# Performance work log

Hardware: AMD Instinct MI355X
Metric: run time of the kernel (lower is better)

The kernel has to match this reference:

```python
import jax, jax.numpy as jnp
import numpy as np

N, E, D, H = 50000, 500000, 128, 128


def setup_inputs() -> dict:
    key = jax.random.key(0)
    ks = jax.random.split(key, 20)
    s = 0.05
    inp = {
        "node_states": jax.random.normal(ks[0], (N, D), jnp.float32),
        "edge_features": jax.random.normal(ks[1], (E, D), jnp.float32),
        "from_idx": jax.random.randint(ks[2], (E,), 0, N, dtype=jnp.int32),
        "to_idx": jax.random.randint(ks[3], (E,), 0, N, dtype=jnp.int32),
        "graph_idx": jax.random.randint(ks[4], (N,), 0, 16, dtype=jnp.int32),
        # message MLP: Linear(3D,H)-ReLU-Linear(H,H)-ReLU-Linear(H,D)
        "mW1": jax.random.normal(ks[5], (3 * D, H), jnp.float32) * s,
        "mb1": jnp.zeros((H,), jnp.float32),
        "mW2": jax.random.normal(ks[6], (H, H), jnp.float32) * s,
        "mb2": jnp.zeros((H,), jnp.float32),
        "mW3": jax.random.normal(ks[7], (H, D), jnp.float32) * s,
        "mb3": jnp.zeros((D,), jnp.float32),
    }
    # three GRU cells; W: input->gates [D,3D], U: hidden->gates [D,3D]; gate order r,z,n (torch)
    for i, g in enumerate(["g0", "g1", "g2"]):
        inp[g + "W"] = jax.random.normal(ks[8 + 2 * i], (D, 3 * D), jnp.float32) * s
        inp[g + "U"] = jax.random.normal(ks[9 + 2 * i], (D, 3 * D), jnp.float32) * s
        inp[g + "b"] = jnp.zeros((3 * D,), jnp.float32)
        inp[g + "c"] = jnp.zeros((3 * D,), jnp.float32)
    return inp


def _mlp(x, W1, b1, W2, b2, W3, b3):
    h = jax.nn.relu(x @ W1 + b1)
    h = jax.nn.relu(h @ W2 + b2)
    return h @ W3 + b3


def _gru(x, h, W, U, b, c):
    gi = x @ W + b  # [N,3D]
    gh = h @ U + c
    ir, iz, inn = jnp.split(gi, 3, axis=1)
    hr, hz, hn = jnp.split(gh, 3, axis=1)
    r = jax.nn.sigmoid(ir + hr)
    z = jax.nn.sigmoid(iz + hz)
    n = jnp.tanh(inn + r * hn)
    return (1.0 - z) * n + z * h


def reference(node_states, edge_features, from_idx, to_idx, graph_idx,
              mW1, mb1, mW2, mb2, mW3, mb3,
              g0W, g0U, g0b, g0c, g1W, g1U, g1b, g1c, g2W, g2U, g2b, g2c):
    n_nodes = node_states.shape[0]

    def prop_once(fi, ti):
        edge_in = jnp.concatenate(
            [node_states[fi], node_states[ti], edge_features], axis=1)  # [E,3D]
        edge_states = _mlp(edge_in, mW1, mb1, mW2, mb2, mW3, mb3)  # [E,D]
        return jax.ops.segment_sum(edge_states, ti, num_segments=n_nodes)

    # forward uses self.message_net for BOTH directions (reverse net unused)
    agg = prop_once(from_idx, to_idx) + prop_once(to_idx, from_idx)  # [N,D]

    h1 = _gru(node_states, agg, g0W, g0U, g0b, g0c)
    h2 = _gru(agg, h1, g1W, g1U, g1b, g1c)
    h3 = _gru(h1, h2, g2W, g2U, g2b, g2c)
    return h3
```

## Files before the change

### kernel.cpp

```cpp
#include <hip/hip_runtime.h>

typedef unsigned short u16;
typedef __attribute__((ext_vector_type(8))) short bf16x8;
typedef __attribute__((ext_vector_type(4))) float f32x4;

__device__ inline u16 f2bf(float f) {
  unsigned int u = __float_as_uint(f);
  u += 0x7fffu + ((u >> 16) & 1u);
  return (u16)(u >> 16);
}
__device__ inline float bf2f(u16 v) {
  return __uint_as_float((unsigned)v << 16);
}

__device__ inline uint4 pack8(float4 a, float4 b) {
  uint4 r;
  r.x = (unsigned)f2bf(a.x) | ((unsigned)f2bf(a.y) << 16);
  r.y = (unsigned)f2bf(a.z) | ((unsigned)f2bf(a.w) << 16);
  r.z = (unsigned)f2bf(b.x) | ((unsigned)f2bf(b.y) << 16);
  r.w = (unsigned)f2bf(b.z) | ((unsigned)f2bf(b.w) << 16);
  return r;
}

struct TransDesc {
  const float* src[9];
  u16* dst[9];
  int R[9];
  int C[9];
  int pre[10];
};

__global__ void transpose_all_kernel(TransDesc td) {
  int t = blockIdx.x * 256 + threadIdx.x;
  if (t >= td.pre[9]) return;
  int seg = 0;
  while (t >= td.pre[seg + 1]) ++seg;
  int local = t - td.pre[seg];
  int C = td.C[seg], R = td.R[seg];
  int r = local / C, c = local - r * C;
  td.dst[seg][(size_t)c * R + r] = f2bf(td.src[seg][local]);
}

__global__ void count_kernel(const int* __restrict__ fi,
                             const int* __restrict__ ti,
                             int* __restrict__ cnt, int E) {
  int e = blockIdx.x * 256 + threadIdx.x;
  if (e < E) {
    atomicAdd(&cnt[ti[e]], 1);
    atomicAdd(&cnt[fi[e]], 1);
  }
}

__global__ void scan1_kernel(const int* __restrict__ cnt,
                             int* __restrict__ partial, int N, int chunk) {
  __shared__ int sdata[256];
  int b = blockIdx.x, t = threadIdx.x;
  int base = b * chunk;
  int sum = 0;
  for (int i = t; i < chunk; i += 256) {
    int idx = base + i;
    if (idx < N) sum += cnt[idx];
  }
  sdata[t] = sum;
  __syncthreads();
  for (int s2 = 128; s2 > 0; s2 >>= 1) {
    if (t < s2) sdata[t] += sdata[t + s2];
    __syncthreads();
  }
  if (t == 0) partial[b] = sdata[0];
}

__global__ void scan2_kernel(int* __restrict__ partial) {
  __shared__ int s[256];
  int t = threadIdx.x;
  int own = partial[t];
  s[t] = own;
  __syncthreads();
  for (int d2 = 1; d2 < 256; d2 <<= 1) {
    int v = (t >= d2) ? s[t - d2] : 0;
    __syncthreads();
    s[t] += v;
    __syncthreads();
  }
  partial[t] = s[t] - own;
}

__global__ void scan3_kernel(const int* __restrict__ cnt,
                             const int* __restrict__ partialEx,
                             int* __restrict__ cursor, int N, int chunk) {
  __shared__ int s[256];
  int b = blockIdx.x, t = threadIdx.x;
  int base = b * chunk;
  int own = (t < chunk && base + t < N) ? cnt[base + t] : 0;
  s[t] = own;
  __syncthreads();
  for (int d2 = 1; d2 < 256; d2 <<= 1) {
    int v = (t >= d2) ? s[t - d2] : 0;
    __syncthreads();
    s[t] += v;
    __syncthreads();
  }
  int ex = s[t] - own + partialEx[b];
  if (t < chunk && base + t < N) cursor[base + t] = ex;
}

__global__ void slot_kernel(const int* __restrict__ fi,
                            const int* __restrict__ ti,
                            int* __restrict__ cursor, int* __restrict__ s_nbr,
                            int* __restrict__ s_eid, int* __restrict__ s_dest,
                            int E) {
  int e = blockIdx.x * 256 + threadIdx.x;
  if (e < E) {
    int f = fi[e], t2 = ti[e];
    int p0 = atomicAdd(&cursor[t2], 1);
    s_nbr[p0] = f;
    s_eid[p0] = e;
    s_dest[p0] = t2;
    int p1 = atomicAdd(&cursor[f], 1);
    s_nbr[p1] = t2;
    s_eid[p1] = e;
    s_dest[p1] = f;
  }
}

__device__ inline void stage_w_rw(u16* sW, const u16* __restrict__ src,
                                  int roww, int colofs, int tid) {
  int n = tid >> 1, half = tid & 1;
  const u16* s = src + (size_t)n * roww + colofs + half * 64;
#pragma unroll
  for (int q = 0; q < 8; ++q) {
    uint4 v = *(const uint4*)(s + q * 8);
    int byte = n * 256 + ((half * 128 + q * 16) ^ ((n & 7) << 4));
    *(uint4*)((char*)sW + byte) = v;
  }
}

__device__ inline void mfma_pass(const u16* A, const u16* W, f32x4 acc[8],
                                 int w, int lane) {
  const int cA = lane & 15;
  const int ko = (lane >> 4) * 8;
  const int arow = 16 * w + cA;
#pragma unroll
  for (int kk = 0; kk < 4; ++kk) {
    int ka = (kk * 32 + ko) * 2;
    int sx = ka ^ ((cA & 7) << 4);
    bf16x8 a = *(const bf16x8*)((const char*)A + arow * 256 + sx);
#pragma unroll
    for (int nt = 0; nt < 8; ++nt) {
      bf16x8 bb = *(const bf16x8*)((const char*)W + (nt * 16 + cA) * 256 + sx);
      acc[nt] = __builtin_amdgcn_mfma_f32_16x16x32_bf16(a, bb, acc[nt], 0, 0, 0);
    }
  }
}

__device__ inline void write_h_lds(u16* sH, const f32x4 acc[8], int w,
                                   int lane) {
#pragma unroll
  for (int nt = 0; nt < 8; ++nt) {
    int col = nt * 16 + (lane & 15);
#pragma unroll
    for (int i = 0; i < 4; ++i) {
      int rr = 16 * w + ((lane >> 4) * 4) + i;
      *(u16*)((char*)sH + rr * 256 + ((col * 2) ^ ((rr & 7) << 4))) =
          f2bf(acc[nt][i]);
    }
  }
}

__global__ __launch_bounds__(256) void node_partial_kernel(
    const float* __restrict__ ns, const u16* __restrict__ Wt1,
    u16* __restrict__ Pa, u16* __restrict__ Pb, int N) {
  __shared__ u16 sA[64 * 128];
  __shared__ u16 sW[128 * 128];
  const int tid = threadIdx.x;
  const int lane = tid & 63;
  const int w = tid >> 6;
  const int r0 = blockIdx.x * 64;
  {
    int row = tid >> 2, seg = tid & 3;
    int rr = r0 + row;
    if (rr >= N) rr = N - 1;
    const float4* sx = (const float4*)(ns + (size_t)rr * 128 + seg * 32);
#pragma unroll
    for (int q = 0; q < 4; ++q) {
      int byte = row * 256 + ((seg * 64 + q * 16) ^ ((row & 7) << 4));
      *(uint4*)((char*)sA + byte) = pack8(sx[q * 2], sx[q * 2 + 1]);
    }
  }
  stage_w_rw(sW, Wt1, 384, 0, tid);
  __syncthreads();
  f32x4 accA[8] = {};
  mfma_pass(sA, sW, accA, w, lane);
  __syncthreads();
  stage_w_rw(sW, Wt1, 384, 128, tid);
  __syncthreads();
  f32x4 accB[8] = {};
  mfma_pass(sA, sW, accB, w, lane);
#pragma unroll
  for (int nt = 0; nt < 8; ++nt) {
    int col = nt * 16 + (lane & 15);
#pragma unroll
    for (int i = 0; i < 4; ++i) {
      int rr = 16 * w + ((lane >> 4) * 4) + i;
      int row = r0 + rr;
      if (row < N) {
        Pa[(size_t)row * 128 + col] = f2bf(accA[nt][i]);
        Pb[(size_t)row * 128 + col] = f2bf(accB[nt][i]);
      }
    }
  }
}

__global__ __launch_bounds__(256) void efgemm_kernel(
    const float* __restrict__ ef, const u16* __restrict__ Wt1,
    const float* __restrict__ b1, u16* __restrict__ EFm, int E) {
  __shared__ u16 sA[64 * 128];
  __shared__ u16 sW[128 * 128];
  const int tid = threadIdx.x;
  const int lane = tid & 63;
  const int w = tid >> 6;
  const int r0 = blockIdx.x * 64;
  {
    int row = tid >> 2, seg = tid & 3;
    int rr = r0 + row;
    if (rr >= E) rr = E - 1;
    const float4* sx = (const float4*)(ef + (size_t)rr * 128 + seg * 32);
#pragma unroll
    for (int q = 0; q < 4; ++q) {
      int byte = row * 256 + ((seg * 64 + q * 16) ^ ((row & 7) << 4));
      *(uint4*)((char*)sA + byte) = pack8(sx[q * 2], sx[q * 2 + 1]);
    }
  }
  stage_w_rw(sW, Wt1, 384, 256, tid);
  __syncthreads();
  f32x4 acc[8] = {};
  mfma_pass(sA, sW, acc, w, lane);
  __syncthreads();
#pragma unroll
  for (int nt = 0; nt < 8; ++nt) {
    int col = nt * 16 + (lane & 15);
    float bv = b1[col];
#pragma unroll
    for (int i = 0; i < 4; ++i) {
      int rr = 16 * w + ((lane >> 4) * 4) + i;
      *(u16*)((char*)sA + rr * 256 + ((col * 2) ^ ((rr & 7) << 4))) =
          f2bf(acc[nt][i] + bv);
    }
  }
  __syncthreads();
#pragma unroll
  for (int it = 0; it < 4; ++it) {
    int task = tid + (it << 8);
    int row = task >> 4, c8 = task & 15;
    int gr = r0 + row;
    if (gr < E) {
      uint4 v = *(const uint4*)((const char*)sA + row * 256 +
                                ((c8 << 4) ^ ((row & 7) << 4)));
      *(uint4*)(EFm + (size_t)gr * 128 + (c8 << 3)) = v;
    }
  }
}

__global__ __launch_bounds__(512, 2) void edge_csr_kernel(
    const u16* __restrict__ EFm, const int* __restrict__ s_nbr,
    const int* __restrict__ s_eid, const int* __restrict__ s_dest,
    const u16* __restrict__ Wt2, const u16* __restrict__ Wt3,
    const u16* __restrict__ Pa, const u16* __restrict__ Pb,
    const float* __restrict__ b2, const float* __restrict__ b3,
    float* __restrict__ aggf, int nslots, int ntiles) {
  __shared__ u16 sH[128 * 128];
  __shared__ int sNbr[128];
  __shared__ int sEid[128];
  __shared__ int sDest[128];
  const int tid = threadIdx.x;
  const int lane = tid & 63;
  const int wv = tid >> 6;
  const int mw = wv >> 1;
  const int nw = wv & 1;
  const int l15 = lane & 15;
  const int lhi = lane >> 4;

  float b2f[4], b3f[4];
#pragma unroll
  for (int nt = 0; nt < 4; ++nt) {
    int col = (nw << 6) + (nt << 4) + l15;
    b2f[nt] = b2[col];
    b3f[nt] = b3[col];
  }
  bf16x8 w2f[4][4], w3f[4][4];
#pragma unroll
  for (int nt = 0; nt < 4; ++nt) {
    int c = (nw << 6) + (nt << 4) + l15;
#pragma unroll
    for (int kk = 0; kk < 4; ++kk) {
      w2f[nt][kk] = *(const bf16x8*)(Wt2 + (size_t)c * 128 + (kk << 5) + (lhi << 3));
      w3f[nt][kk] = *(const bf16x8*)(Wt3 + (size_t)c * 128 + (kk << 5) + (lhi << 3));
    }
  }
  __syncthreads();

  for (int t = blockIdx.x; t < ntiles; t += gridDim.x) {
    const int r0 = t << 7;
    if (tid < 128) {
      int r = r0 + tid;
      int rc = r < nslots ? r : nslots - 1;
      sNbr[tid] = s_nbr[rc];
      sEid[tid] = s_eid[rc];
      sDest[tid] = (r < nslots) ? s_dest[rc] : -1;
    }
    __syncthreads();
#pragma unroll
    for (int it = 0; it < 4; ++it) {
      int row = (tid >> 4) + (it << 5);
      int c8 = tid & 15;
      int nbr = sNbr[row], eid = sEid[row];
      int dst = sDest[row];
      if (dst < 0) dst = 0;
      uint4 efv = *(const uint4*)(EFm + (size_t)eid * 128 + (c8 << 3));
      uint4 pav = *(const uint4*)(Pa + (size_t)nbr * 128 + (c8 << 3));
      uint4 pbv = *(const uint4*)(Pb + (size_t)dst * 128 + (c8 << 3));
      const u16* pe = (const u16*)&efv;
      const u16* pa = (const u16*)&pav;
      const u16* pb = (const u16*)&pbv;
      unsigned o[4];
#pragma unroll
      for (int j = 0; j < 4; ++j) {
        float v0 = fmaxf(bf2f(pe[2 * j]) + bf2f(pa[2 * j]) + bf2f(pb[2 * j]), 0.f);
        float v1 = fmaxf(bf2f(pe[2 * j + 1]) + bf2f(pa[2 * j + 1]) + bf2f(pb[2 * j + 1]), 0.f);
        o[j] = (unsigned)f2bf(v0) | ((unsigned)f2bf(v1) << 16);
      }
      *(uint4*)((char*)sH + row * 256 + ((c8 << 4) ^ ((row & 7) << 4))) = *(uint4*)o;
    }
    __syncthreads();
    bf16x8 hA[2][4];
#pragma unroll
    for (int m = 0; m < 2; ++m) {
      int ra = (mw << 5) + (m << 4) + l15;
#pragma unroll
      for (int kk = 0; kk < 4; ++kk) {
        int sx = ((kk << 6) + (lhi << 4)) ^ ((ra & 7) << 4);
        hA[m][kk] = *(const bf16x8*)((const char*)sH + ra * 256 + sx);
      }
    }
    f32x4 acc2[2][4] = {};
#pragma unroll
    for (int kk = 0; kk < 4; ++kk)
#pragma unroll
      for (int nt = 0; nt < 4; ++nt)
#pragma unroll
        for (int m = 0; m < 2; ++m)
          acc2[m][nt] = __builtin_amdgcn_mfma_f32_16x16x32_bf16(
              hA[m][kk], w2f[nt][kk], acc2[m][nt], 0, 0, 0);
    __syncthreads();
#pragma unroll
    for (int m = 0; m < 2; ++m) {
#pragma unroll
      for (int i = 0; i < 4; ++i) {
        int rl = (mw << 5) + (m << 4) + (lhi << 2) + i;
#pragma unroll
        for (int nt = 0; nt < 4; ++nt) {
          int col = (nw << 6) + (nt << 4) + l15;
          float v = fmaxf(acc2[m][nt][i] + b2f[nt], 0.f);
          *(u16*)((char*)sH + rl * 256 + ((col * 2) ^ ((rl & 7) << 4))) = f2bf(v);
        }
      }
    }
    __syncthreads();
#pragma unroll
    for (int m = 0; m < 2; ++m) {
      int ra = (mw << 5) + (m << 4) + l15;
#pragma unroll
      for (int kk = 0; kk < 4; ++kk) {
        int sx = ((kk << 6) + (lhi << 4)) ^ ((ra & 7) << 4);
        hA[m][kk] = *(const bf16x8*)((const char*)sH + ra * 256 + sx);
      }
    }
    f32x4 acc3[2][4] = {};
#pragma unroll
    for (int kk = 0; kk < 4; ++kk)
#pragma unroll
      for (int nt = 0; nt < 4; ++nt)
#pragma unroll
        for (int m = 0; m < 2; ++m)
          acc3[m][nt] = __builtin_amdgcn_mfma_f32_16x16x32_bf16(
              hA[m][kk], w3f[nt][kk], acc3[m][nt], 0, 0, 0);
    __syncthreads();
#pragma unroll
    for (int m = 0; m < 2; ++m) {
#pragma unroll
      for (int i = 0; i < 4; ++i) {
        int rl = (mw << 5) + (m << 4) + (lhi << 2) + i;
#pragma unroll
        for (int nt = 0; nt < 4; ++nt) {
          int col = (nw << 6) + (nt << 4) + l15;
          *(u16*)((char*)sH + rl * 256 + ((col * 2) ^ ((rl & 7) << 4))) =
              f2bf(acc3[m][nt][i] + b3f[nt]);
        }
      }
    }
    __syncthreads();
    {
      int c = tid & 127, q = tid >> 7;
      float s = 0.f;
      int prev = -1;
      int rbeg = q << 5;
#pragma unroll 4
      for (int rr = rbeg; rr < rbeg + 32; ++rr) {
        int d = sDest[rr];
        if (d != prev) {
          if (prev >= 0) unsafeAtomicAdd(&aggf[(size_t)prev * 128 + c], s);
          prev = d;
          s = 0.f;
        }
        if (d >= 0)
          s += bf2f(*(const u16*)((const char*)sH + rr * 256 +
                                  ((c * 2) ^ ((rr & 7) << 4))));
      }
      if (prev >= 0) unsafeAtomicAdd(&aggf[(size_t)prev * 128 + c], s);
    }
    __syncthreads();
  }
}

__global__ __launch_bounds__(256, 2) void gru3_kernel(
    const float* __restrict__ ns, const float* __restrict__ aggf,
    const u16* __restrict__ g0W, const u16* __restrict__ g0U,
    const u16* __restrict__ g1W, const u16* __restrict__ g1U,
    const u16* __restrict__ g2W, const u16* __restrict__ g2U,
    const float* __restrict__ b0, const float* __restrict__ c0,
    const float* __restrict__ b1, const float* __restrict__ c1,
    const float* __restrict__ b2, const float* __restrict__ c2,
    float* __restrict__ out, int N) {
  __shared__ u16 sX[64 * 128];
  __shared__ u16 sG[64 * 128];
  __shared__ u16 sW[128 * 128];
  const int tid = threadIdx.x;
  const int lane = tid & 63;
  const int w = tid >> 6;
  const int r0 = blockIdx.x * 64;
  {
    int row = tid >> 2, seg = tid & 3;
    int rr = r0 + row;
    if (rr >= N) rr = N - 1;
    const float4* sx = (const float4*)(ns + (size_t)rr * 128 + seg * 32);
    const float4* sh = (const float4*)(aggf + (size_t)rr * 128 + seg * 32);
#pragma unroll
    for (int q = 0; q < 4; ++q) {
      int byte = row * 256 + ((seg * 64 + q * 16) ^ ((row & 7) << 4));
      *(uint4*)((char*)sX + byte) = pack8(sx[q * 2], sx[q * 2 + 1]);
      *(uint4*)((char*)sG + byte) = pack8(sh[q * 2], sh[q * 2 + 1]);
    }
  }

  float hpf[8][4];

#define GPASS(SRC, ABUF, ACC)                       \
  __syncthreads();                                  \
  stage_w_rw(sW, (SRC), 128, 0, tid);               \
  __syncthreads();                                  \
  mfma_pass((ABUF), sW, (ACC), w, lane);

  {
    f32x4 ar[8] = {}, az[8] = {}, ai[8] = {}, ah[8] = {};
    GPASS(g0W + 0 * 16384, sX, ar)
    GPASS(g0U + 0 * 16384, sG, ar)
    GPASS(g0W + 1 * 16384, sX, az)
    GPASS(g0U + 1 * 16384, sG, az)
    GPASS(g0W + 2 * 16384, sX, ai)
    GPASS(g0U + 2 * 16384, sG, ah)
    f32x4 h1[8];
#pragma unroll
    for (int nt = 0; nt < 8; ++nt) {
      int col = nt * 16 + (lane & 15);
      float brc = b0[col] + c0[col];
      float bzc = b0[128 + col] + c0[128 + col];
      float bi = b0[256 + col];
      float bc2 = c0[256 + col];
#pragma unroll
      for (int i = 0; i < 4; ++i) {
        int rloc = 16 * w + ((lane >> 4) * 4) + i;
        int row = r0 + rloc;
        int rowc = row < N ? row : N - 1;
        float hf = aggf[(size_t)rowc * 128 + col];
        float rg = 1.f / (1.f + __expf(-(ar[nt][i] + brc)));
        float zg = 1.f / (1.f + __expf(-(az[nt][i] + bzc)));
        float pre = ai[nt][i] + bi + rg * (ah[nt][i] + bc2);
        float ng = 2.f / (1.f + __expf(-2.f * pre)) - 1.f;
        float hv = (1.f - zg) * ng + zg * hf;
        h1[nt][i] = hv;
        hpf[nt][i] = hv;
      }
    }
    write_h_lds(sX, h1, w, lane);
  }
  {
    f32x4 ar[8] = {}, az[8] = {}, ai[8] = {}, ah[8] = {};
    GPASS(g1W + 0 * 16384, sG, ar)
    GPASS(g1U + 0 * 16384, sX, ar)
    GPASS(g1W + 1 * 16384, sG, az)
    GPASS(g1U + 1 * 16384, sX, az)
    GPASS(g1W + 2 * 16384, sG, ai)
    GPASS(g1U + 2 * 16384, sX, ah)
    f32x4 h2[8];
#pragma unroll
    for (int nt = 0; nt < 8; ++nt) {
      int col = nt * 16 + (lane & 15);
      float brc = b1[col] + c1[col];
      float bzc = b1[128 + col] + c1[128 + col];
      float bi = b1[256 + col];
      float bc2 = c1[256 + col];
#pragma unroll
      for (int i = 0; i < 4; ++i) {
        float rg = 1.f / (1.f + __expf(-(ar[nt][i] + brc)));
        float zg = 1.f / (1.f + __expf(-(az[nt][i] + bzc)));
        float pre = ai[nt][i] + bi + rg * (ah[nt][i] + bc2);
        float ng = 2.f / (1.f + __expf(-2.f * pre)) - 1.f;
        float hv = (1.f - zg) * ng + zg * hpf[nt][i];
        h2[nt][i] = hv;
        hpf[nt][i] = hv;
      }
    }
    write_h_lds(sG, h2, w, lane);
  }
  {
    f32x4 ar[8] = {}, az[8] = {}, ai[8] = {}, ah[8] = {};
    GPASS(g2W + 0 * 16384, sX, ar)
    GPASS(g2U + 0 * 16384, sG, ar)
    GPASS(g2W + 1 * 16384, sX, az)
    GPASS(g2U + 1 * 16384, sG, az)
    GPASS(g2W + 2 * 16384, sX, ai)
    GPASS(g2U + 2 * 16384, sG, ah)
#pragma unroll
    for (int nt = 0; nt < 8; ++nt) {
      int col = nt * 16 + (lane & 15);
      float brc = b2[col] + c2[col];
      float bzc = b2[128 + col] + c2[128 + col];
      float bi = b2[256 + col];
      float bc2 = c2[256 + col];
#pragma unroll
      for (int i = 0; i < 4; ++i) {
        int rloc = 16 * w + ((lane >> 4) * 4) + i;
        int row = r0 + rloc;
        if (row < N) {
          float rg = 1.f / (1.f + __expf(-(ar[nt][i] + brc)));
          float zg = 1.f / (1.f + __expf(-(az[nt][i] + bzc)));
          float pre = ai[nt][i] + bi + rg * (ah[nt][i] + bc2);
          float ng = 2.f / (1.f + __expf(-2.f * pre)) - 1.f;
          out[(size_t)row * 128 + col] = (1.f - zg) * ng + zg * hpf[nt][i];
        }
      }
    }
  }
#undef GPASS
}

extern "C" void kernel_launch(void* const* d_in, const int* in_sizes, int n_in,
                              void* d_out, int out_size, void* d_ws,
                              size_t ws_size, hipStream_t stream) {
  const float* ns = (const float*)d_in[0];
  const float* ef = (const float*)d_in[1];
  const int* from_idx = (const int*)d_in[2];
  const int* to_idx = (const int*)d_in[3];
  const float* mW1 = (const float*)d_in[5];
  const float* mb1 = (const float*)d_in[6];
  const float* mW2 = (const float*)d_in[7];
  const float* mb2 = (const float*)d_in[8];
  const float* mW3 = (const float*)d_in[9];
  const float* mb3 = (const float*)d_in[10];
  const float* gW[3] = {(const float*)d_in[11], (const float*)d_in[15], (const float*)d_in[19]};
  const float* gU[3] = {(const float*)d_in[12], (const float*)d_in[16], (const float*)d_in[20]};
  const float* gb[3] = {(const float*)d_in[13], (const float*)d_in[17], (const float*)d_in[21]};
  const float* gc[3] = {(const float*)d_in[14], (const float*)d_in[18], (const float*)d_in[22]};

  const int N = in_sizes[0] / 128;
  const int E = in_sizes[1] / 128;
  const int nslots = 2 * E;

  char* base = (char*)d_ws;
  size_t cur = 0;
  auto alloc = [&](size_t bytes) {
    size_t p = cur;
    cur = (cur + bytes + 255) & ~(size_t)255;
    return (void*)(base + p);
  };
  float* aggf = (float*)alloc((size_t)N * 128 * 4);
  u16* Pa = (u16*)alloc((size_t)N * 128 * 2);
  u16* Pb = (u16*)alloc((size_t)N * 128 * 2);
  u16* Wt1 = (u16*)alloc(384 * 128 * 2);
  u16* Wt2 = (u16*)alloc(128 * 128 * 2);
  u16* Wt3 = (u16*)alloc(128 * 128 * 2);
  u16 *gWt[3], *gUt[3];
  for (int i = 0; i < 3; ++i) {
    gWt[i] = (u16*)alloc(384 * 128 * 2);
    gUt[i] = (u16*)alloc(384 * 128 * 2);
  }
  int* cnt = (int*)alloc((size_t)N * 4);
  int* cursor = (int*)alloc((size_t)N * 4);
  int* partial = (int*)alloc(256 * 4);
  int* s_nbr = (int*)alloc((size_t)nslots * 4);
  int* s_eid = (int*)alloc((size_t)nslots * 4);
  int* s_dest = (int*)alloc((size_t)nslots * 4);
  u16* EFm = (u16*)alloc((size_t)E * 128 * 2);
  (void)ws_size;

  {
    TransDesc td;
    const float* srcs[9] = {mW1, mW2, mW3, gW[0], gU[0], gW[1], gU[1], gW[2], gU[2]};
    u16* dsts[9] = {Wt1, Wt2, Wt3, gWt[0], gUt[0], gWt[1], gUt[1], gWt[2], gUt[2]};
    int Rs[9] = {384, 128, 128, 128, 128, 128, 128, 128, 128};
    int Cs[9] = {128, 128, 128, 384, 384, 384, 384, 384, 384};
    int acc = 0;
    for (int i = 0; i < 9; ++i) {
      td.src[i] = srcs[i];
      td.dst[i] = dsts[i];
      td.R[i] = Rs[i];
      td.C[i] = Cs[i];
      td.pre[i] = acc;
      acc += Rs[i] * Cs[i];
    }
    td.pre[9] = acc;
    transpose_all_kernel<<<(acc + 255) / 256, 256, 0, stream>>>(td);
  }

  node_partial_kernel<<<(N + 63) / 64, 256, 0, stream>>>(ns, Wt1, Pa, Pb, N);

  hipMemsetAsync(cnt, 0, (size_t)N * 4, stream);
  count_kernel<<<(E + 255) / 256, 256, 0, stream>>>(from_idx, to_idx, cnt, E);
  int chunk = (N + 255) / 256;
  scan1_kernel<<<256, 256, 0, stream>>>(cnt, partial, N, chunk);
  scan2_kernel<<<1, 256, 0, stream>>>(partial);
  scan3_kernel<<<256, 256, 0, stream>>>(cnt, partial, cursor, N, chunk);
  slot_kernel<<<(E + 255) / 256, 256, 0, stream>>>(from_idx, to_idx, cursor,
                                                   s_nbr, s_eid, s_dest, E);

  efgemm_kernel<<<(E + 63) / 64, 256, 0, stream>>>(ef, Wt1, mb1, EFm, E);

  hipMemsetAsync(aggf, 0, (size_t)N * 128 * 4, stream);
  int ntiles = (nslots + 127) / 128;
  int egrid = ntiles < 512 ? ntiles : 512;
  edge_csr_kernel<<<egrid, 512, 0, stream>>>(EFm, s_nbr, s_eid, s_dest, Wt2,
                                             Wt3, Pa, Pb, mb2, mb3, aggf,
                                             nslots, ntiles);

  int gblocks = (N + 63) / 64;
  gru3_kernel<<<gblocks, 256, 0, stream>>>(
      ns, aggf, gWt[0], gUt[0], gWt[1], gUt[1], gWt[2], gUt[2], gb[0], gc[0],
      gb[1], gc[1], gb[2], gc[2], (float*)d_out, N);
}
```

Before: 648.9 us.

## Merge layer-1 GEMMs, stage edge MLP weights in LDS, enlarge GRU tiles

Three unrelated changes. The node-partial and edge-feature GEMMs are merged into one launch that picks its branch by block index, saving a launch and letting both run together. The edge kernel now keeps W2/W3 in shared memory instead of registers, uses 64-row tiles and reads slot indices straight from global memory, freeing registers at the cost of extra LDS traffic. The GRU kernel moves to 512 threads with 128-row tiles and a matching weight-staging helper so each staged weight tile is reused by more rows.

After: 632.3 us. 1.03x faster.

```diff
diff --git a/kernel.cpp b/kernel.cpp
--- a/kernel.cpp
+++ b/kernel.cpp
@@ -135,6 +135,18 @@
   }
 }
 
+__device__ inline void stage_w_512(u16* sW, const u16* __restrict__ src,
+                                   int roww, int colofs, int tid) {
+  int n = tid >> 2, quarter = tid & 3;
+  const u16* s = src + (size_t)n * roww + colofs + quarter * 32;
+#pragma unroll
+  for (int q = 0; q < 4; ++q) {
+    uint4 v = *(const uint4*)(s + q * 8);
+    int byte = n * 256 + ((quarter * 64 + q * 16) ^ ((n & 7) << 4));
+    *(uint4*)((char*)sW + byte) = v;
+  }
+}
+
 __device__ inline void mfma_pass(const u16* A, const u16* W, f32x4 acc[8],
                                  int w, int lane) {
   const int cA = lane & 15;
@@ -167,111 +179,105 @@
   }
 }
 
-__global__ __launch_bounds__(256) void node_partial_kernel(
-    const float* __restrict__ ns, const u16* __restrict__ Wt1,
-    u16* __restrict__ Pa, u16* __restrict__ Pb, int N) {
+__global__ __launch_bounds__(256) void gemm1_kernel(
+    const float* __restrict__ ns, const float* __restrict__ ef,
+    const u16* __restrict__ Wt1, const float* __restrict__ b1,
+    u16* __restrict__ Pa, u16* __restrict__ Pb, u16* __restrict__ EFm, int N,
+    int E, int Nb) {
   __shared__ u16 sA[64 * 128];
   __shared__ u16 sW[128 * 128];
   const int tid = threadIdx.x;
   const int lane = tid & 63;
   const int w = tid >> 6;
-  const int r0 = blockIdx.x * 64;
-  {
-    int row = tid >> 2, seg = tid & 3;
-    int rr = r0 + row;
-    if (rr >= N) rr = N - 1;
-    const float4* sx = (const float4*)(ns + (size_t)rr * 128 + seg * 32);
-#pragma unroll
-    for (int q = 0; q < 4; ++q) {
-      int byte = row * 256 + ((seg * 64 + q * 16) ^ ((row & 7) << 4));
-      *(uint4*)((char*)sA + byte) = pack8(sx[q * 2], sx[q * 2 + 1]);
-    }
-  }
-  stage_w_rw(sW, Wt1, 384, 0, tid);
-  __syncthreads();
-  f32x4 accA[8] = {};
-  mfma_pass(sA, sW, accA, w, lane);
-  __syncthreads();
-  stage_w_rw(sW, Wt1, 384, 128, tid);
-  __syncthreads();
-  f32x4 accB[8] = {};
-  mfma_pass(sA, sW, accB, w, lane);
-#pragma unroll
-  for (int nt = 0; nt < 8; ++nt) {
-    int col = nt * 16 + (lane & 15);
-#pragma unroll
-    for (int i = 0; i < 4; ++i) {
-      int rr = 16 * w + ((lane >> 4) * 4) + i;
-      int row = r0 + rr;
-      if (row < N) {
-        Pa[(size_t)row * 128 + col] = f2bf(accA[nt][i]);
-        Pb[(size_t)row * 128 + col] = f2bf(accB[nt][i]);
-      }
-    }
-  }
-}
-
-__global__ __launch_bounds__(256) void efgemm_kernel(
-    const float* __restrict__ ef, const u16* __restrict__ Wt1,
-    const float* __restrict__ b1, u16* __restrict__ EFm, int E) {
-  __shared__ u16 sA[64 * 128];
-  __shared__ u16 sW[128 * 128];
-  const int tid = threadIdx.x;
-  const int lane = tid & 63;
-  const int w = tid >> 6;
-  const int r0 = blockIdx.x * 64;
-  {
-    int row = tid >> 2, seg = tid & 3;
-    int rr = r0 + row;
-    if (rr >= E) rr = E - 1;
-    const float4* sx = (const float4*)(ef + (size_t)rr * 128 + seg * 32);
-#pragma unroll
-    for (int q = 0; q < 4; ++q) {
-      int byte = row * 256 + ((seg * 64 + q * 16) ^ ((row & 7) << 4));
-      *(uint4*)((char*)sA + byte) = pack8(sx[q * 2], sx[q * 2 + 1]);
-    }
-  }
-  stage_w_rw(sW, Wt1, 384, 256, tid);
-  __syncthreads();
-  f32x4 acc[8] = {};
-  mfma_pass(sA, sW, acc, w, lane);
-  __syncthreads();
-#pragma unroll
-  for (int nt = 0; nt < 8; ++nt) {
-    int col = nt * 16 + (lane & 15);
-    float bv = b1[col];
-#pragma unroll
-    for (int i = 0; i < 4; ++i) {
-      int rr = 16 * w + ((lane >> 4) * 4) + i;
-      *(u16*)((char*)sA + rr * 256 + ((col * 2) ^ ((rr & 7) << 4))) =
-          f2bf(acc[nt][i] + bv);
-    }
-  }
-  __syncthreads();
-#pragma unroll
-  for (int it = 0; it < 4; ++it) {
-    int task = tid + (it << 8);
-    int row = task >> 4, c8 = task & 15;
-    int gr = r0 + row;
-    if (gr < E) {
-      uint4 v = *(const uint4*)((const char*)sA + row * 256 +
-                                ((c8 << 4) ^ ((row & 7) << 4)));
-      *(uint4*)(EFm + (size_t)gr * 128 + (c8 << 3)) = v;
-    }
-  }
-}
-
-__global__ __launch_bounds__(512, 2) void edge_csr_kernel(
+  if ((int)blockIdx.x < Nb) {
+    const int r0 = blockIdx.x * 64;
+    {
+      int row = tid >> 2, seg = tid & 3;
+      int rr = r0 + row;
+      if (rr >= N) rr = N - 1;
+      const float4* sx = (const float4*)(ns + (size_t)rr * 128 + seg * 32);
+#pragma unroll
+      for (int q = 0; q < 4; ++q) {
+        int byte = row * 256 + ((seg * 64 + q * 16) ^ ((row & 7) << 4));
+        *(uint4*)((char*)sA + byte) = pack8(sx[q * 2], sx[q * 2 + 1]);
+      }
+    }
+    stage_w_rw(sW, Wt1, 384, 0, tid);
+    __syncthreads();
+    f32x4 accA[8] = {};
+    mfma_pass(sA, sW, accA, w, lane);
+    __syncthreads();
+    stage_w_rw(sW, Wt1, 384, 128, tid);
+    __syncthreads();
+    f32x4 accB[8] = {};
+    mfma_pass(sA, sW, accB, w, lane);
+#pragma unroll
+    for (int nt = 0; nt < 8; ++nt) {
+      int col = nt * 16 + (lane & 15);
+#pragma unroll
+      for (int i = 0; i < 4; ++i) {
+        int rr = 16 * w + ((lane >> 4) * 4) + i;
+        int row = r0 + rr;
+        if (row < N) {
+          Pa[(size_t)row * 128 + col] = f2bf(accA[nt][i]);
+          Pb[(size_t)row * 128 + col] = f2bf(accB[nt][i]);
+        }
+      }
+    }
+  } else {
+    const int r0 = (blockIdx.x - Nb) * 64;
+    {
+      int row = tid >> 2, seg = tid & 3;
+      int rr = r0 + row;
+      if (rr >= E) rr = E - 1;
+      const float4* sx = (const float4*)(ef + (size_t)rr * 128 + seg * 32);
+#pragma unroll
+      for (int q = 0; q < 4; ++q) {
+        int byte = row * 256 + ((seg * 64 + q * 16) ^ ((row & 7) << 4));
+        *(uint4*)((char*)sA + byte) = pack8(sx[q * 2], sx[q * 2 + 1]);
+      }
+    }
+    stage_w_rw(sW, Wt1, 384, 256, tid);
+    __syncthreads();
+    f32x4 acc[8] = {};
+    mfma_pass(sA, sW, acc, w, lane);
+    __syncthreads();
+#pragma unroll
+    for (int nt = 0; nt < 8; ++nt) {
+      int col = nt * 16 + (lane & 15);
+      float bv = b1[col];
+#pragma unroll
+      for (int i = 0; i < 4; ++i) {
+        int rr = 16 * w + ((lane >> 4) * 4) + i;
+        *(u16*)((char*)sA + rr * 256 + ((col * 2) ^ ((rr & 7) << 4))) =
+            f2bf(acc[nt][i] + bv);
+      }
+    }
+    __syncthreads();
+#pragma unroll
+    for (int it = 0; it < 4; ++it) {
+      int task = tid + (it << 8);
+      int row = task >> 4, c8 = task & 15;
+      int gr = r0 + row;
+      if (gr < E) {
+        uint4 v = *(const uint4*)((const char*)sA + row * 256 +
+                                  ((c8 << 4) ^ ((row & 7) << 4)));
+        *(uint4*)(EFm + (size_t)gr * 128 + (c8 << 3)) = v;
+      }
+    }
+  }
+}
+
+__global__ __launch_bounds__(512, 2) void edge_csr2_kernel(
     const u16* __restrict__ EFm, const int* __restrict__ s_nbr,
     const int* __restrict__ s_eid, const int* __restrict__ s_dest,
     const u16* __restrict__ Wt2, const u16* __restrict__ Wt3,
     const u16* __restrict__ Pa, const u16* __restrict__ Pb,
     const float* __restrict__ b2, const float* __restrict__ b3,
     float* __restrict__ aggf, int nslots, int ntiles) {
-  __shared__ u16 sH[128 * 128];
-  __shared__ int sNbr[128];
-  __shared__ int sEid[128];
-  __shared__ int sDest[128];
+  __shared__ u16 sW2[128 * 128];
+  __shared__ u16 sW3[128 * 128];
+  __shared__ u16 sH[64 * 128];
   const int tid = threadIdx.x;
   const int lane = tid & 63;
   const int wv = tid >> 6;
@@ -280,6 +286,8 @@
   const int l15 = lane & 15;
   const int lhi = lane >> 4;
 
+  stage_w_512(sW2, Wt2, 128, 0, tid);
+  stage_w_512(sW3, Wt3, 128, 0, tid);
   float b2f[4], b3f[4];
 #pragma unroll
   for (int nt = 0; nt < 4; ++nt) {
@@ -287,35 +295,20 @@
     b2f[nt] = b2[col];
     b3f[nt] = b3[col];
   }
-  bf16x8 w2f[4][4], w3f[4][4];
-#pragma unroll
-  for (int nt = 0; nt < 4; ++nt) {
-    int c = (nw << 6) + (nt << 4) + l15;
-#pragma unroll
-    for (int kk = 0; kk < 4; ++kk) {
-      w2f[nt][kk] = *(const bf16x8*)(Wt2 + (size_t)c * 128 + (kk << 5) + (lhi << 3));
-      w3f[nt][kk] = *(const bf16x8*)(Wt3 + (size_t)c * 128 + (kk << 5) + (lhi << 3));
-    }
-  }
   __syncthreads();
 
+  const int ra = (mw << 4) + l15;
+
   for (int t = blockIdx.x; t < ntiles; t += gridDim.x) {
-    const int r0 = t << 7;
-    if (tid < 128) {
-      int r = r0 + tid;
+    const int r0 = t << 6;
+#pragma unroll
+    for (int it = 0; it < 2; ++it) {
+      int task = tid + (it << 9);
+      int row = task >> 4;
+      int c8 = task & 15;
+      int r = r0 + row;
       int rc = r < nslots ? r : nslots - 1;
-      sNbr[tid] = s_nbr[rc];
-      sEid[tid] = s_eid[rc];
-      sDest[tid] = (r < nslots) ? s_dest[rc] : -1;
-    }
-    __syncthreads();
-#pragma unroll
-    for (int it = 0; it < 4; ++it) {
-      int row = (tid >> 4) + (it << 5);
-      int c8 = tid & 15;
-      int nbr = sNbr[row], eid = sEid[row];
-      int dst = sDest[row];
-      if (dst < 0) dst = 0;
+      int nbr = s_nbr[rc], eid = s_eid[rc], dst = s_dest[rc];
       uint4 efv = *(const uint4*)(EFm + (size_t)eid * 128 + (c8 << 3));
       uint4 pav = *(const uint4*)(Pa + (size_t)nbr * 128 + (c8 << 3));
       uint4 pbv = *(const uint4*)(Pb + (size_t)dst * 128 + (c8 << 3));
@@ -332,70 +325,60 @@
       *(uint4*)((char*)sH + row * 256 + ((c8 << 4) ^ ((row & 7) << 4))) = *(uint4*)o;
     }
     __syncthreads();
-    bf16x8 hA[2][4];
-#pragma unroll
-    for (int m = 0; m < 2; ++m) {
-      int ra = (mw << 5) + (m << 4) + l15;
-#pragma unroll
-      for (int kk = 0; kk < 4; ++kk) {
-        int sx = ((kk << 6) + (lhi << 4)) ^ ((ra & 7) << 4);
-        hA[m][kk] = *(const bf16x8*)((const char*)sH + ra * 256 + sx);
-      }
-    }
-    f32x4 acc2[2][4] = {};
-#pragma unroll
-    for (int kk = 0; kk < 4; ++kk)
-#pragma unroll
-      for (int nt = 0; nt < 4; ++nt)
-#pragma unroll
-        for (int m = 0; m < 2; ++m)
-          acc2[m][nt] = __builtin_amdgcn_mfma_f32_16x16x32_bf16(
-              hA[m][kk], w2f[nt][kk], acc2[m][nt], 0, 0, 0);
-    __syncthreads();
-#pragma unroll
-    for (int m = 0; m < 2; ++m) {
-#pragma unroll
-      for (int i = 0; i < 4; ++i) {
-        int rl = (mw << 5) + (m << 4) + (lhi << 2) + i;
-#pragma unroll
-        for (int nt = 0; nt < 4; ++nt) {
-          int col = (nw << 6) + (nt << 4) + l15;
-          float v = fmaxf(acc2[m][nt][i] + b2f[nt], 0.f);
-          *(u16*)((char*)sH + rl * 256 + ((col * 2) ^ ((rl & 7) << 4))) = f2bf(v);
-        }
-      }
-    }
-    __syncthreads();
-#pragma unroll
-    for (int m = 0; m < 2; ++m) {
-      int ra = (mw << 5) + (m << 4) + l15;
-#pragma unroll
-      for (int kk = 0; kk < 4; ++kk) {
-        int sx = ((kk << 6) + (lhi << 4)) ^ ((ra & 7) << 4);
-        hA[m][kk] = *(const bf16x8*)((const char*)sH + ra * 256 + sx);
-      }
-    }
-    f32x4 acc3[2][4] = {};
-#pragma unroll
-    for (int kk = 0; kk < 4; ++kk)
-#pragma unroll
-      for (int nt = 0; nt < 4; ++nt)
-#pragma unroll
-        for (int m = 0; m < 2; ++m)
-          acc3[m][nt] = __builtin_amdgcn_mfma_f32_16x16x32_bf16(
-              hA[m][kk], w3f[nt][kk], acc3[m][nt], 0, 0, 0);
-    __syncthreads();
-#pragma unroll
-    for (int m = 0; m < 2; ++m) {
-#pragma unroll
-      for (int i = 0; i < 4; ++i) {
-        int rl = (mw << 5) + (m << 4) + (lhi << 2) + i;
-#pragma unroll
-        for (int nt = 0; nt < 4; ++nt) {
-          int col = (nw << 6) + (nt << 4) + l15;
-          *(u16*)((char*)sH + rl * 256 + ((col * 2) ^ ((rl & 7) << 4))) =
-              f2bf(acc3[m][nt][i] + b3f[nt]);
-        }
+    bf16x8 hA[4];
+#pragma unroll
+    for (int kk = 0; kk < 4; ++kk) {
+      int sx = ((kk << 6) + (lhi << 4)) ^ ((ra & 7) << 4);
+      hA[kk] = *(const bf16x8*)((const char*)sH + ra * 256 + sx);
+    }
+    f32x4 acc[4] = {};
+#pragma unroll
+    for (int kk = 0; kk < 4; ++kk) {
+#pragma unroll
+      for (int nt = 0; nt < 4; ++nt) {
+        int c = (nw << 6) + (nt << 4) + l15;
+        int sx = ((kk << 6) + (lhi << 4)) ^ ((c & 7) << 4);
+        bf16x8 bb = *(const bf16x8*)((const char*)sW2 + c * 256 + sx);
+        acc[nt] = __builtin_amdgcn_mfma_f32_16x16x32_bf16(hA[kk], bb, acc[nt], 0, 0, 0);
+      }
+    }
+    __syncthreads();
+#pragma unroll
+    for (int i = 0; i < 4; ++i) {
+      int rl = (mw << 4) + (lhi << 2) + i;
+#pragma unroll
+      for (int nt = 0; nt < 4; ++nt) {
+        int col = (nw << 6) + (nt << 4) + l15;
+        float v = fmaxf(acc[nt][i] + b2f[nt], 0.f);
+        *(u16*)((char*)sH + rl * 256 + ((col * 2) ^ ((rl & 7) << 4))) = f2bf(v);
+        acc[nt][i] = 0.f;
+      }
+    }
+    __syncthreads();
+#pragma unroll
+    for (int kk = 0; kk < 4; ++kk) {
+      int sx = ((kk << 6) + (lhi << 4)) ^ ((ra & 7) << 4);
+      hA[kk] = *(const bf16x8*)((const char*)sH + ra * 256 + sx);
+    }
+#pragma unroll
+    for (int kk = 0; kk < 4; ++kk) {
+#pragma unroll
+      for (int nt = 0; nt < 4; ++nt) {
+        int c = (nw << 6) + (nt << 4) + l15;
+        int sx = ((kk << 6) + (lhi << 4)) ^ ((c & 7) << 4);
+        bf16x8 bb = *(const bf16x8*)((const char*)sW3 + c * 256 + sx);
+        acc[nt] = __builtin_amdgcn_mfma_f32_16x16x32_bf16(hA[kk], bb, acc[nt], 0, 0, 0);
+      }
+    }
+    __syncthreads();
+#pragma unroll
+    for (int i = 0; i < 4; ++i) {
+      int rl = (mw << 4) + (lhi << 2) + i;
+#pragma unroll
+      for (int nt = 0; nt < 4; ++nt) {
+        int col = (nw << 6) + (nt << 4) + l15;
+        *(u16*)((char*)sH + rl * 256 + ((col * 2) ^ ((rl & 7) << 4))) =
+            f2bf(acc[nt][i] + b3f[nt]);
       }
     }
     __syncthreads();
@@ -403,10 +386,11 @@
       int c = tid & 127, q = tid >> 7;
       float s = 0.f;
       int prev = -1;
-      int rbeg = q << 5;
+      int rbeg = q << 4;
 #pragma unroll 4
-      for (int rr = rbeg; rr < rbeg + 32; ++rr) {
-        int d = sDest[rr];
+      for (int rr = rbeg; rr < rbeg + 16; ++rr) {
+        int r = r0 + rr;
+        int d = (r < nslots) ? s_dest[r] : -1;
         if (d != prev) {
           if (prev >= 0) unsafeAtomicAdd(&aggf[(size_t)prev * 128 + c], s);
           prev = d;
@@ -422,7 +406,7 @@
   }
 }
 
-__global__ __launch_bounds__(256, 2) void gru3_kernel(
+__global__ __launch_bounds__(512, 1) void gru3_kernel(
     const float* __restrict__ ns, const float* __restrict__ aggf,
     const u16* __restrict__ g0W, const u16* __restrict__ g0U,
     const u16* __restrict__ g1W, const u16* __restrict__ g1U,
@@ -431,13 +415,13 @@
     const float* __restrict__ b1, const float* __restrict__ c1,
     const float* __restrict__ b2, const float* __restrict__ c2,
     float* __restrict__ out, int N) {
-  __shared__ u16 sX[64 * 128];
-  __shared__ u16 sG[64 * 128];
+  __shared__ u16 sX[128 * 128];
+  __shared__ u16 sG[128 * 128];
   __shared__ u16 sW[128 * 128];
   const int tid = threadIdx.x;
   const int lane = tid & 63;
   const int w = tid >> 6;
-  const int r0 = blockIdx.x * 64;
+  const int r0 = blockIdx.x * 128;
   {
     int row = tid >> 2, seg = tid & 3;
     int rr = r0 + row;
@@ -456,7 +440,7 @@
 
 #define GPASS(SRC, ABUF, ACC)                       \
   __syncthreads();                                  \
-  stage_w_rw(sW, (SRC), 128, 0, tid);               \
+  stage_w_512(sW, (SRC), 128, 0, tid);              \
   __syncthreads();                                  \
   mfma_pass((ABUF), sW, (ACC), w, lane);
 
@@ -622,8 +606,6 @@
     transpose_all_kernel<<<(acc + 255) / 256, 256, 0, stream>>>(td);
   }
 
-  node_partial_kernel<<<(N + 63) / 64, 256, 0, stream>>>(ns, Wt1, Pa, Pb, N);
-
   hipMemsetAsync(cnt, 0, (size_t)N * 4, stream);
   count_kernel<<<(E + 255) / 256, 256, 0, stream>>>(from_idx, to_idx, cnt, E);
   int chunk = (N + 255) / 256;
@@ -633,17 +615,19 @@
   slot_kernel<<<(E + 255) / 256, 256, 0, stream>>>(from_idx, to_idx, cursor,
                                                    s_nbr, s_eid, s_dest, E);
 
-  efgemm_kernel<<<(E + 63) / 64, 256, 0, stream>>>(ef, Wt1, mb1, EFm, E);
+  int Nb = (N + 63) / 64, Eb = (E + 63) / 64;
+  gemm1_kernel<<<Nb + Eb, 256, 0, stream>>>(ns, ef, Wt1, mb1, Pa, Pb, EFm, N,
+                                            E, Nb);
 
   hipMemsetAsync(aggf, 0, (size_t)N * 128 * 4, stream);
-  int ntiles = (nslots + 127) / 128;
+  int ntiles = (nslots + 63) / 64;
   int egrid = ntiles < 512 ? ntiles : 512;
-  edge_csr_kernel<<<egrid, 512, 0, stream>>>(EFm, s_nbr, s_eid, s_dest, Wt2,
-                                             Wt3, Pa, Pb, mb2, mb3, aggf,
-                                             nslots, ntiles);
-
-  int gblocks = (N + 63) / 64;
-  gru3_kernel<<<gblocks, 256, 0, stream>>>(
+  edge_csr2_kernel<<<egrid, 512, 0, stream>>>(EFm, s_nbr, s_eid, s_dest, Wt2,
+                                              Wt3, Pa, Pb, mb2, mb3, aggf,
+                                              nslots, ntiles);
+
+  int gblocks = (N + 127) / 128;
+  gru3_kernel<<<gblocks, 512, 0, stream>>>(
       ns, aggf, gWt[0], gUt[0], gWt[1], gUt[1], gWt[2], gUt[2], gb[0], gc[0],
       gb[1], gc[1], gb[2], gc[2], (float*)d_out, N);
 }
```
